# Optimization experiments

Hardware: AMD Instinct MI355X
Metric: run time of the kernel (lower is better)

## Reference

```python
import jax, jax.numpy as jnp
import numpy as np

jax.config.update("jax_enable_x64", True)  # hash arithmetic needs 64-bit ints

P = 56598313          # RzLinear.P (prime for the hash)
INPUT_DIM = 4096
OUTPUT_DIM = 4096
COMPRESS_RATIO = 0.0625
HASH_SIZE = int(INPUT_DIM * OUTPUT_DIM * COMPRESS_RATIO)  # 1,048,576
N_TOKENS = 8192


def setup_inputs() -> dict:
    key = jax.random.key(0)
    kx, kw, kr = jax.random.split(key, 3)
    x = jax.random.normal(kx, (N_TOKENS, INPUT_DIM), dtype=jnp.float32)
    hashed_weight = jax.random.normal(kw, (HASH_SIZE,), dtype=jnp.float32) * 0.02
    # _generate_random_numbers: [P, r1, r2, r3] with r_i forced even via r + r % 2
    r = jax.random.randint(kr, (3,), 0, P, dtype=jnp.int64)
    r = r + r % 2
    random_numbers = jnp.concatenate([jnp.array([P], dtype=jnp.int64), r])
    bias = jnp.zeros((OUTPUT_DIM,), dtype=jnp.float32)
    return {"x": x, "hashed_weight": hashed_weight,
            "random_numbers": random_numbers, "bias": bias}


def _hash_indices(random_numbers):
    # ROBE-Z hash (chunk_size=1): idx[k, n] = ((k*r3 + n*r2 + r1) % P) % HASH_SIZE
    r0 = random_numbers[0]
    r1 = random_numbers[1]
    r2 = random_numbers[2]
    r3 = random_numbers[3]
    k = jnp.arange(INPUT_DIM, dtype=jnp.int64)[:, None]   # (K, 1)
    n = jnp.arange(OUTPUT_DIM, dtype=jnp.int64)[None, :]  # (1, N)
    return ((k * r3 + n * r2 + r1) % r0) % HASH_SIZE       # (K, N)


def reference(x, hashed_weight, random_numbers, bias):
    idx = _hash_indices(random_numbers)
    W = hashed_weight[idx]          # gather-reconstructed (input_dim, output_dim)
    return x @ W + bias             # (N_TOKENS, output_dim)
```

## Files before the change

kernel.cpp:

```cpp
#include <hip/hip_runtime.h>
#include <stdint.h>


#define P_CONST 56598313u
#define HASH_MASK 0xFFFFFu
#define M_DIM 8192
#define N_DIM 4096
#define K_DIM 4096
#define BK 32
#define KSTEPS (K_DIM / BK)

typedef __attribute__((ext_vector_type(8))) short bf16x8;
typedef __attribute__((ext_vector_type(4))) float f32x4;

__device__ __forceinline__ unsigned short f2bf(float f) {
    unsigned int u = __float_as_uint(f);
    return (unsigned short)((u + 0x7FFFu + ((u >> 16) & 1u)) >> 16);
}

struct RN { unsigned long long r1, r2, r3; };

__device__ __forceinline__ RN decode_rn(const void* rn_raw) {
    RN o;
    const long long* rn64 = (const long long*)rn_raw;
    if (rn64[0] == 56598313LL) {
        o.r1 = (unsigned long long)rn64[1];
        o.r2 = (unsigned long long)rn64[2];
        o.r3 = (unsigned long long)rn64[3];
    } else {
        const int* rn32 = (const int*)rn_raw;
        o.r1 = (unsigned long long)(unsigned int)rn32[1];
        o.r2 = (unsigned long long)(unsigned int)rn32[2];
        o.r3 = (unsigned long long)(unsigned int)rn32[3];
    }
    return o;
}

__device__ __forceinline__ void load16(const void* g, void* l) {
    __builtin_amdgcn_global_load_lds(
        (const __attribute__((address_space(1))) void*)g,
        (__attribute__((address_space(3))) void*)l,
        16, 0, 0);
}

__global__ __launch_bounds__(256) void build_wt(const float* __restrict__ table,
                                                const void* __restrict__ rn_raw,
                                                unsigned short* __restrict__ Wt) {
    RN rn = decode_rn(rn_raw);
    const unsigned int stepu = (unsigned int)(rn.r3 % P_CONST);
    const unsigned int n = blockIdx.x;
    const unsigned long long base =
        ((unsigned long long)n * rn.r2 + rn.r1) % P_CONST;
    const int t = threadIdx.x;
#pragma unroll
    for (int e = 0; e < 2; ++e) {
        const int k0 = (t + e * 256) * 8;
        unsigned int cur =
            (unsigned int)((base + (unsigned long long)k0 * stepu) % P_CONST);
        union { unsigned short s[8]; uint4 v; } o;
#pragma unroll
        for (int i = 0; i < 8; ++i) {
            o.s[i] = f2bf(table[cur & HASH_MASK]);
            cur += stepu;
            if (cur >= P_CONST) cur -= P_CONST;
        }
        *(uint4*)(Wt + (size_t)n * K_DIM + k0) = o.v;
    }
}

__global__ __launch_bounds__(256) void cvt_x(const float* __restrict__ x,
                                             unsigned short* __restrict__ xb) {
    const size_t i8 = ((size_t)blockIdx.x * 256 + threadIdx.x) * 8;
    const float4 a = *(const float4*)(x + i8);
    const float4 b = *(const float4*)(x + i8 + 4);
    union { unsigned short s[8]; uint4 v; } o;
    o.s[0] = f2bf(a.x); o.s[1] = f2bf(a.y); o.s[2] = f2bf(a.z); o.s[3] = f2bf(a.w);
    o.s[4] = f2bf(b.x); o.s[5] = f2bf(b.y); o.s[6] = f2bf(b.z); o.s[7] = f2bf(b.w);
    *(uint4*)(xb + i8) = o.v;
}

__global__ __launch_bounds__(512, 2) void gemm_bt8(
    const unsigned short* __restrict__ A,
    const unsigned short* __restrict__ Bt,
    const float* __restrict__ bias,
    float* __restrict__ C) {
    __shared__ __align__(16) unsigned short lA[4][256 * BK];
    __shared__ __align__(16) unsigned short lB[4][256 * BK];

    const int t = threadIdx.x;
    const int bid0 = blockIdx.x;
    const int sb = (bid0 & 7) * 64 + (bid0 >> 3);
    const int m0 = (sb >> 4) * 256;
    const int n0 = (sb & 15) * 256;

    const int lane = t & 63;
    const int wid = t >> 6;
    const int wr = wid >> 2;
    const int wc = wid & 3;
    const int lm = lane & 15;
    const int q = lane >> 4;
    const int qswz = (q ^ ((lm >> 1) & 3)) << 4;

    const int p0 = t * 16;
    const int p1 = p0 + 8192;
    const int l0 = p0 ^ ((p0 >> 3) & 0x30);
    const int l1 = p1 ^ ((p1 >> 3) & 0x30);
    const int r0 = l0 >> 6, c0 = (l0 & 63) >> 1;
    const int r1 = l1 >> 6, c1 = (l1 & 63) >> 1;

    const unsigned short* Abase = A + (size_t)m0 * K_DIM;
    const unsigned short* Bbase = Bt + (size_t)n0 * K_DIM;

    f32x4 acc[8][4] = {};

#define STAGE_A(KS) do { const int b__ = (KS) & 3;                              \
    load16(Abase + (size_t)r0 * K_DIM + (KS) * BK + c0, (char*)&lA[b__][0] + p0);\
    load16(Abase + (size_t)r1 * K_DIM + (KS) * BK + c1, (char*)&lA[b__][0] + p1);\
} while (0)
#define STAGE_B(KS) do { const int b__ = (KS) & 3;                              \
    load16(Bbase + (size_t)r0 * K_DIM + (KS) * BK + c0, (char*)&lB[b__][0] + p0);\
    load16(Bbase + (size_t)r1 * K_DIM + (KS) * BK + c1, (char*)&lB[b__][0] + p1);\
} while (0)

#define STEP_BODY(KS, STG) do {                                                 \
    __builtin_amdgcn_s_barrier();                                               \
    asm volatile("" ::: "memory");                                              \
    const char* bufA = (const char*)&lA[(KS) & 3][0];                           \
    const char* bufB = (const char*)&lB[(KS) & 3][0];                           \
    bf16x8 af[4], bfr[4];                                                       \
    _Pragma("unroll")                                                           \
    for (int i = 0; i < 4; ++i)                                                 \
        af[i] = *(const bf16x8*)(bufA + (((wr * 128 + i * 16 + lm) << 6) | qswz));\
    _Pragma("unroll")                                                           \
    for (int j = 0; j < 4; ++j)                                                 \
        bfr[j] = *(const bf16x8*)(bufB + (((wc * 64 + j * 16 + lm) << 6) | qswz));\
    if (STG) STAGE_A((KS) + 3);                                                 \
    asm volatile("s_waitcnt lgkmcnt(0)" ::: "memory");                          \
    __builtin_amdgcn_sched_barrier(0);                                          \
    __builtin_amdgcn_s_setprio(1);                                              \
    _Pragma("unroll")                                                           \
    for (int i = 0; i < 4; ++i)                                                 \
        _Pragma("unroll")                                                       \
        for (int j = 0; j < 4; ++j)                                             \
            acc[i][j] = __builtin_amdgcn_mfma_f32_16x16x32_bf16(                \
                af[i], bfr[j], acc[i][j], 0, 0, 0);                             \
    __builtin_amdgcn_s_setprio(0);                                              \
    __builtin_amdgcn_s_barrier();                                               \
    asm volatile("" ::: "memory");                                              \
    _Pragma("unroll")                                                           \
    for (int i = 0; i < 4; ++i)                                                 \
        af[i] = *(const bf16x8*)(bufA + (((wr * 128 + 64 + i * 16 + lm) << 6) | qswz));\
    if (STG) STAGE_B((KS) + 3);                                                 \
    asm volatile("s_waitcnt lgkmcnt(0)" ::: "memory");                          \
    __builtin_amdgcn_sched_barrier(0);                                          \
    __builtin_amdgcn_s_setprio(1);                                              \
    _Pragma("unroll")                                                           \
    for (int i = 0; i < 4; ++i)                                                 \
        _Pragma("unroll")                                                       \
        for (int j = 0; j < 4; ++j)                                             \
            acc[i + 4][j] = __builtin_amdgcn_mfma_f32_16x16x32_bf16(            \
                af[i], bfr[j], acc[i + 4][j], 0, 0, 0);                         \
    __builtin_amdgcn_s_setprio(0);                                              \
} while (0)

    STAGE_A(0); STAGE_B(0);
    STAGE_A(1); STAGE_B(1);
    STAGE_A(2); STAGE_B(2);

#pragma unroll 1
    for (int ks = 0; ks < KSTEPS - 2; ++ks) {
        asm volatile("s_waitcnt vmcnt(8)" ::: "memory");
        STEP_BODY(ks, (ks < KSTEPS - 3));
    }
    asm volatile("s_waitcnt vmcnt(4)" ::: "memory");
    STEP_BODY(KSTEPS - 2, false);
    asm volatile("s_waitcnt vmcnt(0)" ::: "memory");
    STEP_BODY(KSTEPS - 1, false);

#undef STEP_BODY
#undef STAGE_A
#undef STAGE_B

#pragma unroll
    for (int j = 0; j < 4; ++j) {
        const int col = n0 + wc * 64 + j * 16 + lm;
        const float bv = bias[col];
#pragma unroll
        for (int i = 0; i < 8; ++i) {
            const int row = m0 + wr * 128 + i * 16 + q * 4;
#pragma unroll
            for (int r = 0; r < 4; ++r)
                C[(size_t)(row + r) * N_DIM + col] = acc[i][j][r] + bv;
        }
    }
}

__global__ __launch_bounds__(256) void gemm_fused(const float* __restrict__ X,
                                                  const float* __restrict__ table,
                                                  const void* __restrict__ rn_raw,
                                                  const float* __restrict__ bias,
                                                  float* __restrict__ C) {
    RN rn = decode_rn(rn_raw);
    const unsigned int stepu = (unsigned int)(rn.r3 % P_CONST);
    const unsigned int step32 =
        (unsigned int)(((unsigned long long)stepu * 32ull) % P_CONST);

    __shared__ __align__(16) unsigned short lA[128 * 32];
    __shared__ __align__(16) unsigned short lB[128 * 32];
    const int t = threadIdx.x;
    const int m0 = blockIdx.y * 128;
    const int n0 = blockIdx.x * 128;
    const int lane = t & 63;
    const int w = t >> 6;
    const int wr = w >> 1, wc = w & 1;
    const int lm = lane & 15, q = lane >> 4;

    unsigned int curB[2];
    int rowB[2], colB[2];
#pragma unroll
    for (int e = 0; e < 2; ++e) {
        const int c = t + e * 256;
        rowB[e] = c >> 2;
        colB[e] = (c & 3) * 8;
        const unsigned long long base =
            ((unsigned long long)(n0 + rowB[e]) * rn.r2 + rn.r1) % P_CONST;
        curB[e] =
            (unsigned int)((base + (unsigned long long)colB[e] * stepu) % P_CONST);
    }

    f32x4 acc[4][4] = {};

    for (int k0 = 0; k0 < K_DIM; k0 += 32) {
#pragma unroll
        for (int c = t; c < 1024; c += 256) {
            const int row = c >> 3, col = (c & 7) * 4;
            const float4 v =
                *(const float4*)(X + (size_t)(m0 + row) * K_DIM + k0 + col);
            ushort4 o;
            o.x = f2bf(v.x); o.y = f2bf(v.y); o.z = f2bf(v.z); o.w = f2bf(v.w);
            *(ushort4*)&lA[row * 32 + col] = o;
        }
#pragma unroll
        for (int e = 0; e < 2; ++e) {
            unsigned int cur = curB[e];
            union { unsigned short s[8]; uint4 v; } o;
#pragma unroll
            for (int i = 0; i < 8; ++i) {
                o.s[i] = f2bf(table[cur & HASH_MASK]);
                cur += stepu;
                if (cur >= P_CONST) cur -= P_CONST;
            }
            curB[e] += step32;
            if (curB[e] >= P_CONST) curB[e] -= P_CONST;
            *(uint4*)&lB[rowB[e] * 32 + colB[e]] = o.v;
        }
        __syncthreads();

        bf16x8 af[4], bfr[4];
#pragma unroll
        for (int i = 0; i < 4; ++i)
            af[i] = *(const bf16x8*)&lA[(wr * 64 + i * 16 + lm) * 32 + q * 8];
#pragma unroll
        for (int j = 0; j < 4; ++j)
            bfr[j] = *(const bf16x8*)&lB[(wc * 64 + j * 16 + lm) * 32 + q * 8];
#pragma unroll
        for (int i = 0; i < 4; ++i)
#pragma unroll
            for (int j = 0; j < 4; ++j)
                acc[i][j] = __builtin_amdgcn_mfma_f32_16x16x32_bf16(
                    af[i], bfr[j], acc[i][j], 0, 0, 0);
        __syncthreads();
    }

#pragma unroll
    for (int j = 0; j < 4; ++j) {
        const int col = n0 + wc * 64 + j * 16 + lm;
        const float bv = bias[col];
#pragma unroll
        for (int i = 0; i < 4; ++i) {
            const int row = m0 + wr * 64 + i * 16 + q * 4;
#pragma unroll
            for (int r = 0; r < 4; ++r)
                C[(size_t)(row + r) * N_DIM + col] = acc[i][j][r] + bv;
        }
    }
}

extern "C" void kernel_launch(void* const* d_in, const int* in_sizes, int n_in,
                              void* d_out, int out_size, void* d_ws, size_t ws_size,
                              hipStream_t stream) {
    const float* x = (const float*)d_in[0];
    const float* hw = (const float*)d_in[1];
    const void* rn = d_in[2];
    const float* bias = (const float*)d_in[3];
    float* out = (float*)d_out;

    const size_t wt_bytes = (size_t)N_DIM * K_DIM * 2;
    const size_t xb_bytes = (size_t)M_DIM * K_DIM * 2;

    if (ws_size >= wt_bytes + xb_bytes) {
        unsigned short* Wt = (unsigned short*)d_ws;
        unsigned short* Xb = (unsigned short*)((char*)d_ws + wt_bytes);
        build_wt<<<N_DIM, 256, 0, stream>>>(hw, rn, Wt);
        cvt_x<<<(M_DIM * K_DIM) / (8 * 256), 256, 0, stream>>>(x, Xb);
        gemm_bt8<<<dim3((M_DIM / 256) * (N_DIM / 256)), 512, 0, stream>>>(Xb, Wt, bias, out);
    } else {
        gemm_fused<<<dim3(N_DIM / 128, M_DIM / 128), 256, 0, stream>>>(x, hw, rn, bias, out);
    }
}
```

Before: 534.7 us.

## Merge weight build and x conversion into one prep kernel; single-phase GEMM step

Fuses the hashed-weight gather and the x-to-bf16 conversion into one interleaved launch, so the gather blocks (one in five) overlap with streaming conversion blocks, and adds nontemporal loads and stores. In the GEMM it loads all eight A fragments at once and issues both A and B stage loads together, removing the mid-step barrier and the second LDS wait phase. The output stores also become nontemporal. This raises register pressure in the GEMM (8 A fragments live at once) and reduces the interleaving between LDS reads and MFMA work.

```diff
diff --git a/kernel.cpp b/kernel.cpp
--- a/kernel.cpp
+++ b/kernel.cpp
@@ -12,6 +12,7 @@
 
 typedef __attribute__((ext_vector_type(8))) short bf16x8;
 typedef __attribute__((ext_vector_type(4))) float f32x4;
+typedef __attribute__((ext_vector_type(4))) unsigned int u32x4;
 
 __device__ __forceinline__ unsigned short f2bf(float f) {
     unsigned int u = __float_as_uint(f);
@@ -43,40 +44,48 @@
         16, 0, 0);
 }
 
-__global__ __launch_bounds__(256) void build_wt(const float* __restrict__ table,
-                                                const void* __restrict__ rn_raw,
-                                                unsigned short* __restrict__ Wt) {
-    RN rn = decode_rn(rn_raw);
-    const unsigned int stepu = (unsigned int)(rn.r3 % P_CONST);
-    const unsigned int n = blockIdx.x;
-    const unsigned long long base =
-        ((unsigned long long)n * rn.r2 + rn.r1) % P_CONST;
+__global__ __launch_bounds__(256) void prep(const float* __restrict__ x,
+                                            const float* __restrict__ table,
+                                            const void* __restrict__ rn_raw,
+                                            unsigned short* __restrict__ Wt,
+                                            unsigned short* __restrict__ Xb) {
+    const int b = blockIdx.x;
     const int t = threadIdx.x;
-#pragma unroll
-    for (int e = 0; e < 2; ++e) {
-        const int k0 = (t + e * 256) * 8;
-        unsigned int cur =
+    if (b % 5 == 0) {
+        RN rn = decode_rn(rn_raw);
+        const unsigned int stepu = (unsigned int)(rn.r3 % P_CONST);
+        const unsigned int n = (unsigned int)(b / 5);
+        const unsigned long long base =
+            ((unsigned long long)n * rn.r2 + rn.r1) % P_CONST;
+        const int k0 = t * 8;
+        unsigned int c0 =
             (unsigned int)((base + (unsigned long long)k0 * stepu) % P_CONST);
-        union { unsigned short s[8]; uint4 v; } o;
+        unsigned int c1 =
+            (unsigned int)((base + (unsigned long long)(k0 + 2048) * stepu) % P_CONST);
+        float f[16];
 #pragma unroll
         for (int i = 0; i < 8; ++i) {
-            o.s[i] = f2bf(table[cur & HASH_MASK]);
-            cur += stepu;
-            if (cur >= P_CONST) cur -= P_CONST;
-        }
-        *(uint4*)(Wt + (size_t)n * K_DIM + k0) = o.v;
-    }
-}
-
-__global__ __launch_bounds__(256) void cvt_x(const float* __restrict__ x,
-                                             unsigned short* __restrict__ xb) {
-    const size_t i8 = ((size_t)blockIdx.x * 256 + threadIdx.x) * 8;
-    const float4 a = *(const float4*)(x + i8);
-    const float4 b = *(const float4*)(x + i8 + 4);
-    union { unsigned short s[8]; uint4 v; } o;
-    o.s[0] = f2bf(a.x); o.s[1] = f2bf(a.y); o.s[2] = f2bf(a.z); o.s[3] = f2bf(a.w);
-    o.s[4] = f2bf(b.x); o.s[5] = f2bf(b.y); o.s[6] = f2bf(b.z); o.s[7] = f2bf(b.w);
-    *(uint4*)(xb + i8) = o.v;
+            f[i] = table[c0 & HASH_MASK];
+            c0 += stepu; if (c0 >= P_CONST) c0 -= P_CONST;
+            f[8 + i] = table[c1 & HASH_MASK];
+            c1 += stepu; if (c1 >= P_CONST) c1 -= P_CONST;
+        }
+        union { unsigned short s[8]; u32x4 v; } o0, o1;
+#pragma unroll
+        for (int i = 0; i < 8; ++i) { o0.s[i] = f2bf(f[i]); o1.s[i] = f2bf(f[8 + i]); }
+        unsigned short* dst = Wt + (size_t)n * K_DIM + k0;
+        __builtin_nontemporal_store(o0.v, (u32x4*)dst);
+        __builtin_nontemporal_store(o1.v, (u32x4*)(dst + 2048));
+    } else {
+        const int cb = b - b / 5 - 1;
+        const size_t i8 = ((size_t)cb * 256 + t) * 8;
+        const f32x4 a = __builtin_nontemporal_load((const f32x4*)(x + i8));
+        const f32x4 c = __builtin_nontemporal_load((const f32x4*)(x + i8 + 4));
+        union { unsigned short s[8]; u32x4 v; } o;
+        o.s[0] = f2bf(a.x); o.s[1] = f2bf(a.y); o.s[2] = f2bf(a.z); o.s[3] = f2bf(a.w);
+        o.s[4] = f2bf(c.x); o.s[5] = f2bf(c.y); o.s[6] = f2bf(c.z); o.s[7] = f2bf(c.w);
+        __builtin_nontemporal_store(o.v, (u32x4*)(Xb + i8));
+    }
 }
 
 __global__ __launch_bounds__(512, 2) void gemm_bt8(
@@ -127,40 +136,24 @@
     asm volatile("" ::: "memory");                                              \
     const char* bufA = (const char*)&lA[(KS) & 3][0];                           \
     const char* bufB = (const char*)&lB[(KS) & 3][0];                           \
-    bf16x8 af[4], bfr[4];                                                       \
+    bf16x8 af[8], bfr[4];                                                       \
     _Pragma("unroll")                                                           \
-    for (int i = 0; i < 4; ++i)                                                 \
+    for (int i = 0; i < 8; ++i)                                                 \
         af[i] = *(const bf16x8*)(bufA + (((wr * 128 + i * 16 + lm) << 6) | qswz));\
     _Pragma("unroll")                                                           \
     for (int j = 0; j < 4; ++j)                                                 \
         bfr[j] = *(const bf16x8*)(bufB + (((wc * 64 + j * 16 + lm) << 6) | qswz));\
-    if (STG) STAGE_A((KS) + 3);                                                 \
+    if (STG) { STAGE_A((KS) + 3); STAGE_B((KS) + 3); }                          \
     asm volatile("s_waitcnt lgkmcnt(0)" ::: "memory");                          \
     __builtin_amdgcn_sched_barrier(0);                                          \
     __builtin_amdgcn_s_setprio(1);                                              \
     _Pragma("unroll")                                                           \
-    for (int i = 0; i < 4; ++i)                                                 \
+    for (int i = 0; i < 8; ++i)                                                 \
         _Pragma("unroll")                                                       \
         for (int j = 0; j < 4; ++j)                                             \
             acc[i][j] = __builtin_amdgcn_mfma_f32_16x16x32_bf16(                \
                 af[i], bfr[j], acc[i][j], 0, 0, 0);                             \
     __builtin_amdgcn_s_setprio(0);                                              \
-    __builtin_amdgcn_s_barrier();                                               \
-    asm volatile("" ::: "memory");                                              \
-    _Pragma("unroll")                                                           \
-    for (int i = 0; i < 4; ++i)                                                 \
-        af[i] = *(const bf16x8*)(bufA + (((wr * 128 + 64 + i * 16 + lm) << 6) | qswz));\
-    if (STG) STAGE_B((KS) + 3);                                                 \
-    asm volatile("s_waitcnt lgkmcnt(0)" ::: "memory");                          \
-    __builtin_amdgcn_sched_barrier(0);                                          \
-    __builtin_amdgcn_s_setprio(1);                                              \
-    _Pragma("unroll")                                                           \
-    for (int i = 0; i < 4; ++i)                                                 \
-        _Pragma("unroll")                                                       \
-        for (int j = 0; j < 4; ++j)                                             \
-            acc[i + 4][j] = __builtin_amdgcn_mfma_f32_16x16x32_bf16(            \
-                af[i], bfr[j], acc[i + 4][j], 0, 0, 0);                         \
-    __builtin_amdgcn_s_setprio(0);                                              \
 } while (0)
 
     STAGE_A(0); STAGE_B(0);
@@ -190,7 +183,8 @@
             const int row = m0 + wr * 128 + i * 16 + q * 4;
 #pragma unroll
             for (int r = 0; r < 4; ++r)
-                C[(size_t)(row + r) * N_DIM + col] = acc[i][j][r] + bv;
+                __builtin_nontemporal_store(
+                    acc[i][j][r] + bv, &C[(size_t)(row + r) * N_DIM + col]);
         }
     }
 }
@@ -301,8 +295,7 @@
     if (ws_size >= wt_bytes + xb_bytes) {
         unsigned short* Wt = (unsigned short*)d_ws;
         unsigned short* Xb = (unsigned short*)((char*)d_ws + wt_bytes);
-        build_wt<<<N_DIM, 256, 0, stream>>>(hw, rn, Wt);
-        cvt_x<<<(M_DIM * K_DIM) / (8 * 256), 256, 0, stream>>>(x, Xb);
+        prep<<<20480, 256, 0, stream>>>(x, hw, rn, Wt, Xb);
         gemm_bt8<<<dim3((M_DIM / 256) * (N_DIM / 256)), 512, 0, stream>>>(Xb, Wt, bias, out);
     } else {
         gemm_fused<<<dim3(N_DIM / 128, M_DIM / 128), 256, 0, stream>>>(x, hw, rn, bias, out);
```

After: 556.3 us. 1.04x slower.
